# Kernel tuning notes

Measured on AMD Instinct MI355X. Metric: run time of the kernel, lower is better.

The kernel has to match this reference:

```python
import jax, jax.numpy as jnp
import numpy as np

D = 64        # state dim (num_output)
H = 256       # MLP hidden width
B = 4096      # batch
NUM_STEPS = 16  # fixed-step Dormand-Prince steps over t in [0,1] per bijector


def _mlp(t, y, W1, b1, W2, b2, W3, b3):
    # time-conditioned MLP: concat scalar t to state, two tanh layers, linear out
    tcol = jnp.full((y.shape[0], 1), t, dtype=y.dtype)
    h = jnp.tanh(jnp.concatenate([y, tcol], axis=1) @ W1 + b1)
    h = jnp.tanh(h @ W2 + b2)
    return h @ W3 + b3


def _dopri5_fixed(f, y0):
    # classic Dormand-Prince (RK45) Butcher tableau, 5th-order solution,
    # fixed step h = 1/NUM_STEPS from t=0 to t=1
    h = jnp.asarray(1.0 / NUM_STEPS, dtype=y0.dtype)

    def step(y, i):
        t = i.astype(y0.dtype) * h
        k1 = f(t, y)
        k2 = f(t + h * (1/5),  y + h * ((1/5) * k1))
        k3 = f(t + h * (3/10), y + h * ((3/40) * k1 + (9/40) * k2))
        k4 = f(t + h * (4/5),  y + h * ((44/45) * k1 - (56/15) * k2 + (32/9) * k3))
        k5 = f(t + h * (8/9),  y + h * ((19372/6561) * k1 - (25360/2187) * k2
                                        + (64448/6561) * k3 - (212/729) * k4))
        k6 = f(t + h,          y + h * ((9017/3168) * k1 - (355/33) * k2
                                        + (46732/5247) * k3 + (49/176) * k4
                                        - (5103/18656) * k5))
        y_next = y + h * ((35/384) * k1 + (500/1113) * k3 + (125/192) * k4
                          - (2187/6784) * k5 + (11/84) * k6)
        return y_next, None

    y_final, _ = jax.lax.scan(step, y0, jnp.arange(NUM_STEPS))
    return y_final


def setup_inputs() -> dict:
    key = jax.random.key(0)
    ks = jax.random.split(key, 7)
    s_in = 1.0 / np.sqrt(D + 1)
    s_h = 1.0 / np.sqrt(H)
    inp = {"x": jax.random.normal(ks[0], (B, D), dtype=jnp.float32)}
    for i, base in enumerate([1, 4]):
        inp[f"p{i}_W1"] = jax.random.normal(ks[base], (D + 1, H), dtype=jnp.float32) * s_in
        inp[f"p{i}_b1"] = jnp.zeros((H,), dtype=jnp.float32)
        inp[f"p{i}_W2"] = jax.random.normal(ks[base + 1], (H, H), dtype=jnp.float32) * s_h
        inp[f"p{i}_b2"] = jnp.zeros((H,), dtype=jnp.float32)
        inp[f"p{i}_W3"] = jax.random.normal(ks[base + 2], (H, D), dtype=jnp.float32) * s_h
        inp[f"p{i}_b3"] = jnp.zeros((D,), dtype=jnp.float32)
    return inp


def reference(x, p0_W1, p0_b1, p0_W2, p0_b2, p0_W3, p0_b3,
              p1_W1, p1_b1, p1_W2, p1_b2, p1_W3, p1_b3):
    # Chain(list(reversed(bijectors))).forward applies bijector 0 first, then 1.
    # FFJORD bijector forward = integrate dz/dt = mlp(t, z) from t=0 to t=1.
    y = x
    params = [(p0_W1, p0_b1, p0_W2, p0_b2, p0_W3, p0_b3),
              (p1_W1, p1_b1, p1_W2, p1_b2, p1_W3, p1_b3)]
    for (W1, b1, W2, b2, W3, b3) in params:
        f = lambda t, z: _mlp(t, z, W1, b1, W2, b2, W3, b3)
        y = _dopri5_fixed(f, y)
    return y
```

## Files before the change

### kernel.cpp

```cpp
#include <hip/hip_runtime.h>

typedef __attribute__((ext_vector_type(8))) short short8;
typedef __attribute__((ext_vector_type(4))) float f32x4;

#define MROWS 16
#define NSTEPS 16


__device__ __forceinline__ unsigned short bf16rne(float f) {
  unsigned int u = __float_as_uint(f);
  u += 0x7FFFu + ((u >> 16) & 1u);
  return (unsigned short)(u >> 16);
}

__device__ __forceinline__ float tanh_fast(float x) {
  x = fminf(12.0f, x);
  float e = __builtin_amdgcn_exp2f(x * 2.8853900817779268f);
  return __builtin_fmaf(-2.0f, __builtin_amdgcn_rcpf(e + 1.0f), 1.0f);
}

__global__ void ffjord_setup(const float* __restrict__ W1a, const float* __restrict__ W2a,
                             const float* __restrict__ W3a, const float* __restrict__ W1b,
                             const float* __restrict__ W2b, const float* __restrict__ W3b,
                             unsigned short* __restrict__ ws) {
  int gid = blockIdx.x * blockDim.x + threadIdx.x;
  int bij = gid / 12288;
  int r = gid - bij * 12288;
  const float* W1 = bij ? W1b : W1a;
  const float* W2 = bij ? W2b : W2a;
  const float* W3 = bij ? W3b : W3a;
  unsigned short* o = ws + bij * 98304;
  const float* src;
  int kstride;
  if (r < 2048) {
    int lane = r & 63, nt = (r >> 6) & 15, ks = r >> 10;
    int k0 = ks * 32 + (lane >> 4) * 8, n = nt * 16 + (lane & 15);
    src = W1 + k0 * 256 + n; kstride = 256; o += r * 8;
  } else if (r < 10240) {
    int rr = r - 2048;
    int lane = rr & 63, nt = (rr >> 6) & 15, ks = rr >> 10;
    int k0 = ks * 32 + (lane >> 4) * 8, n = nt * 16 + (lane & 15);
    src = W2 + k0 * 256 + n; kstride = 256; o += 16384 + rr * 8;
  } else {
    int rr = r - 10240;
    int lane = rr & 63, nt = (rr >> 6) & 3, ks = rr >> 8;
    int k0 = ks * 32 + (lane >> 4) * 8, n = nt * 16 + (lane & 15);
    src = W3 + k0 * 64 + n; kstride = 64; o += 81920 + rr * 8;
  }
  #pragma unroll
  for (int j = 0; j < 8; j++) o[j] = bf16rne(src[j * kstride]);
}

__global__ __launch_bounds__(512, 2) void ffjord_main(
    const float* __restrict__ x, float* __restrict__ out,
    const unsigned short* __restrict__ ws,
    const float* __restrict__ W1a, const float* __restrict__ b1a,
    const float* __restrict__ b2a, const float* __restrict__ b3a,
    const float* __restrict__ W1b, const float* __restrict__ b1b,
    const float* __restrict__ b2b, const float* __restrict__ b3b) {
  __shared__ __align__(16) unsigned short zA[1024];
  __shared__ __align__(16) unsigned short h1A[4096];
  __shared__ __align__(16) unsigned short h2A[4096];
  __shared__ __align__(16) float fbufA[16 * 68];
  __shared__ __align__(16) float fbufB[16 * 68];

  const int tid = threadIdx.x;
  const int wave = tid >> 6;
  const int lane = tid & 63;
  const int cl = lane & 15;
  const int qd = lane >> 4;
  const int w4 = wave & 3;
  const int ksb = (wave >> 2) * 4;
  const int row0 = blockIdx.x * MROWS;
  const int rown = tid >> 5;
  const int d0 = (tid & 31) * 2;

  const float hstep = 1.0f / 16.0f;

  float y[2];
  {
    float2 v = *(const float2*)(x + (row0 + rown) * 64 + d0);
    y[0] = v.x; y[1] = v.y;
  }
  float k[6][2];

  const int zoff = (d0 >> 5) * 512 + (rown + 16 * ((d0 & 31) >> 3)) * 8 + (d0 & 7);

  const float ACO[6][5] = {
      {0.f, 0.f, 0.f, 0.f, 0.f},
      {1.f / 5.f, 0.f, 0.f, 0.f, 0.f},
      {3.f / 40.f, 9.f / 40.f, 0.f, 0.f, 0.f},
      {44.f / 45.f, -56.f / 15.f, 32.f / 9.f, 0.f, 0.f},
      {19372.f / 6561.f, -25360.f / 2187.f, 64448.f / 6561.f, -212.f / 729.f, 0.f},
      {9017.f / 3168.f, -355.f / 33.f, 46732.f / 5247.f, 49.f / 176.f, -5103.f / 18656.f}};
  const float CT[6] = {0.0f, 0.2f, 0.3f, 0.8f, 8.0f / 9.0f, 1.0f};
  const float BW0 = 35.f / 384.f, BW2 = 500.f / 1113.f, BW3 = 125.f / 192.f,
              BW4 = -2187.f / 6784.f, BW5 = 11.f / 84.f;

  for (int bij = 0; bij < 2; bij++) {
    const unsigned short* wsb = ws + bij * 98304;
    const float* W1 = bij ? W1b : W1a;
    const float* b1 = bij ? b1b : b1a;
    const float* b2 = bij ? b2b : b2a;
    const float* b3 = bij ? b3b : b3a;

    float b1c[2], w1tc[2], b2r[2];
    #pragma unroll
    for (int j = 0; j < 2; j++) {
      int c = (wave * 2 + j) * 16 + cl;
      b1c[j] = b1[c];
      w1tc[j] = W1[64 * 256 + c];
      b2r[j] = b2[c];
    }
    float b3r = (wave < 4) ? b3[w4 * 16 + cl] : 0.0f;

    const short8* w1p = (const short8*)wsb;
    const short8* w2p = (const short8*)(wsb + 16384);
    const short8* w3p = (const short8*)(wsb + 81920);
    short8 w1f[2][2];
    #pragma unroll
    for (int ks = 0; ks < 2; ks++)
      #pragma unroll
      for (int j = 0; j < 2; j++)
        w1f[ks][j] = w1p[(ks * 16 + wave * 2 + j) * 64 + lane];
    short8 w2f[8][2];
    #pragma unroll
    for (int ks = 0; ks < 8; ks++)
      #pragma unroll
      for (int j = 0; j < 2; j++)
        w2f[ks][j] = w2p[(ks * 16 + wave * 2 + j) * 64 + lane];
    short8 w3f[4];
    #pragma unroll
    for (int kk = 0; kk < 4; kk++)
      w3f[kk] = w3p[((ksb + kk) * 4 + w4) * 64 + lane];

    for (int step = 0; step < NSTEPS; step++) {
      float stepf = (float)step;
      #pragma unroll
      for (int s = 0; s < 6; s++) {
        float ts = (stepf + CT[s]) * hstep;

        {
          float z0 = y[0], z1 = y[1];
          #pragma unroll
          for (int j = 0; j < 5; j++)
            if (j < s) {
              float a = hstep * ACO[s][j];
              z0 += a * k[j][0];
              z1 += a * k[j][1];
            }
          ushort2 p;
          p.x = bf16rne(z0); p.y = bf16rne(z1);
          *(ushort2*)(zA + zoff) = p;
        }
        __syncthreads();

        {
          short8 a0 = ((const short8*)zA)[lane];
          short8 a1 = ((const short8*)zA)[64 + lane];
          #pragma unroll
          for (int j = 0; j < 2; j++) {
            f32x4 acc = {0.f, 0.f, 0.f, 0.f};
            acc = __builtin_amdgcn_mfma_f32_16x16x32_bf16(a0, w1f[0][j], acc, 0, 0, 0);
            acc = __builtin_amdgcn_mfma_f32_16x16x32_bf16(a1, w1f[1][j], acc, 0, 0, 0);
            int c = (wave * 2 + j) * 16 + cl;
            float be = __builtin_fmaf(ts, w1tc[j], b1c[j]);
            int boff = (c >> 5) * 512 + ((c & 31) >> 3) * 128 + (c & 7);
            #pragma unroll
            for (int reg = 0; reg < 4; reg++)
              h1A[boff + (4 * qd + reg) * 8] = bf16rne(tanh_fast(acc[reg] + be));
          }
        }
        __syncthreads();

        {
          f32x4 zero = {0.f, 0.f, 0.f, 0.f};
          f32x4 acc2[2] = {zero, zero};
          #pragma unroll
          for (int ks = 0; ks < 8; ks++) {
            short8 a = ((const short8*)h1A)[ks * 64 + lane];
            acc2[0] = __builtin_amdgcn_mfma_f32_16x16x32_bf16(a, w2f[ks][0], acc2[0], 0, 0, 0);
            acc2[1] = __builtin_amdgcn_mfma_f32_16x16x32_bf16(a, w2f[ks][1], acc2[1], 0, 0, 0);
          }
          #pragma unroll
          for (int j = 0; j < 2; j++) {
            int c = (wave * 2 + j) * 16 + cl;
            int boff = (c >> 5) * 512 + ((c & 31) >> 3) * 128 + (c & 7);
            #pragma unroll
            for (int reg = 0; reg < 4; reg++)
              h2A[boff + (4 * qd + reg) * 8] = bf16rne(tanh_fast(acc2[j][reg] + b2r[j]));
          }
        }
        __syncthreads();

        {
          f32x4 acc3 = {0.f, 0.f, 0.f, 0.f};
          #pragma unroll
          for (int kk = 0; kk < 4; kk++) {
            short8 a = ((const short8*)h2A)[(ksb + kk) * 64 + lane];
            acc3 = __builtin_amdgcn_mfma_f32_16x16x32_bf16(a, w3f[kk], acc3, 0, 0, 0);
          }
          int c = w4 * 16 + cl;
          float* fb = (wave < 4) ? fbufA : fbufB;
          #pragma unroll
          for (int reg = 0; reg < 4; reg++)
            fb[(4 * qd + reg) * 68 + c] = acc3[reg] + b3r;
        }
        __syncthreads();

        {
          float2 va = *(const float2*)(fbufA + rown * 68 + d0);
          float2 vb = *(const float2*)(fbufB + rown * 68 + d0);
          k[s][0] = va.x + vb.x;
          k[s][1] = va.y + vb.y;
        }
      }

      #pragma unroll
      for (int i = 0; i < 2; i++) {
        float d = BW0 * k[0][i] + BW2 * k[2][i] + BW3 * k[3][i] +
                  BW4 * k[4][i] + BW5 * k[5][i];
        y[i] += hstep * d;
      }
    }
  }

  float2 o2; o2.x = y[0]; o2.y = y[1];
  *(float2*)(out + (row0 + rown) * 64 + d0) = o2;
}

extern "C" void kernel_launch(void* const* d_in, const int* in_sizes, int n_in,
                              void* d_out, int out_size, void* d_ws, size_t ws_size,
                              hipStream_t stream) {
  (void)in_sizes; (void)n_in; (void)out_size; (void)ws_size;
  const float* x   = (const float*)d_in[0];
  const float* W1a = (const float*)d_in[1];
  const float* b1a = (const float*)d_in[2];
  const float* W2a = (const float*)d_in[3];
  const float* b2a = (const float*)d_in[4];
  const float* W3a = (const float*)d_in[5];
  const float* b3a = (const float*)d_in[6];
  const float* W1b = (const float*)d_in[7];
  const float* b1b = (const float*)d_in[8];
  const float* W2b = (const float*)d_in[9];
  const float* b2b = (const float*)d_in[10];
  const float* W3b = (const float*)d_in[11];
  const float* b3b = (const float*)d_in[12];
  unsigned short* ws = (unsigned short*)d_ws;
  float* out = (float*)d_out;

  hipLaunchKernelGGL(ffjord_setup, dim3(96), dim3(256), 0, stream,
                     W1a, W2a, W3a, W1b, W2b, W3b, ws);
  hipLaunchKernelGGL(ffjord_main, dim3(256), dim3(512), 0, stream,
                     x, out, ws, W1a, b1a, b2a, b3a, W1b, b1b, b2b, b3b);
}
```

Baseline: 348.0 us.

## Swap MFMA operand order to transpose outputs, vectorize bf16 packing and LDS stores

Swaps the A/B operands of the MFMA calls so each lane holds four consecutive hidden columns of one row. This allows packed bf16 conversion (cvt_pk_bf16 when available) and 8-byte LDS stores in place of four scalar 2-byte stores. Biases and the time-column term are folded into the accumulator init, and the K-loops are split into two independent accumulator chains to shorten MFMA dependency latency. The z buffer is padded to reduce LDS bank conflicts. The tanh input clamp is removed, which risks inf/NaN for large positive inputs.

```diff
diff --git a/kernel.cpp b/kernel.cpp
--- a/kernel.cpp
+++ b/kernel.cpp
@@ -3,9 +3,7 @@
 typedef __attribute__((ext_vector_type(8))) short short8;
 typedef __attribute__((ext_vector_type(4))) float f32x4;
 
-#define MROWS 16
 #define NSTEPS 16
-
 
 __device__ __forceinline__ unsigned short bf16rne(float f) {
   unsigned int u = __float_as_uint(f);
@@ -13,8 +11,24 @@
   return (unsigned short)(u >> 16);
 }
 
+#if __has_builtin(__builtin_amdgcn_cvt_pk_bf16_f32)
+typedef __attribute__((ext_vector_type(2))) __bf16 v2bf16;
+__device__ __forceinline__ unsigned int pk2(float a, float b) {
+  v2bf16 t = __builtin_amdgcn_cvt_pk_bf16_f32(a, b);
+  unsigned int r;
+  __builtin_memcpy(&r, &t, 4);
+  return r;
+}
+#else
+__device__ __forceinline__ unsigned int pk2(float a, float b) {
+  unsigned int ua = __float_as_uint(a), ub = __float_as_uint(b);
+  ua += 0x7FFFu + ((ua >> 16) & 1u);
+  ub += 0x7FFFu + ((ub >> 16) & 1u);
+  return (ua >> 16) | (ub & 0xFFFF0000u);
+}
+#endif
+
 __device__ __forceinline__ float tanh_fast(float x) {
-  x = fminf(12.0f, x);
   float e = __builtin_amdgcn_exp2f(x * 2.8853900817779268f);
   return __builtin_fmaf(-2.0f, __builtin_amdgcn_rcpf(e + 1.0f), 1.0f);
 }
@@ -58,33 +72,41 @@
     const float* __restrict__ b2a, const float* __restrict__ b3a,
     const float* __restrict__ W1b, const float* __restrict__ b1b,
     const float* __restrict__ b2b, const float* __restrict__ b3b) {
-  __shared__ __align__(16) unsigned short zA[1024];
+  __shared__ __align__(16) unsigned short zA[1088];
   __shared__ __align__(16) unsigned short h1A[4096];
   __shared__ __align__(16) unsigned short h2A[4096];
-  __shared__ __align__(16) float fbufA[16 * 68];
-  __shared__ __align__(16) float fbufB[16 * 68];
+  __shared__ __align__(16) float fbuf[2][16 * 68];
 
   const int tid = threadIdx.x;
   const int wave = tid >> 6;
   const int lane = tid & 63;
   const int cl = lane & 15;
   const int qd = lane >> 4;
-  const int w4 = wave & 3;
-  const int ksb = (wave >> 2) * 4;
-  const int row0 = blockIdx.x * MROWS;
-  const int rown = tid >> 5;
+  const int kh = wave >> 2;
+  const int mt3 = wave & 3;
+  const int c3 = mt3 * 16 + qd * 4;
+  const int row0 = blockIdx.x * 16;
+  const int row = tid >> 5;
   const int d0 = (tid & 31) * 2;
+
+  const int zoff = ((d0 >> 5) * 4 + ((d0 >> 3) & 3)) * 136 + row * 8 + (d0 & 7);
+  const int zrb = qd * 136 + cl * 8;
+
+  int hoff[2];
+  #pragma unroll
+  for (int t = 0; t < 2; t++) {
+    int c0 = (wave * 2 + t) * 16 + qd * 4;
+    hoff[t] = (c0 >> 5) * 512 + ((c0 & 31) >> 3) * 128 + cl * 8 + (c0 & 7);
+  }
 
   const float hstep = 1.0f / 16.0f;
 
   float y[2];
   {
-    float2 v = *(const float2*)(x + (row0 + rown) * 64 + d0);
+    float2 v = *(const float2*)(x + (row0 + row) * 64 + d0);
     y[0] = v.x; y[1] = v.y;
   }
   float k[6][2];
-
-  const int zoff = (d0 >> 5) * 512 + (rown + 16 * ((d0 & 31) >> 3)) * 8 + (d0 & 7);
 
   const float ACO[6][5] = {
       {0.f, 0.f, 0.f, 0.f, 0.f},
@@ -104,15 +126,17 @@
     const float* b2 = bij ? b2b : b2a;
     const float* b3 = bij ? b3b : b3a;
 
-    float b1c[2], w1tc[2], b2r[2];
-    #pragma unroll
-    for (int j = 0; j < 2; j++) {
-      int c = (wave * 2 + j) * 16 + cl;
-      b1c[j] = b1[c];
-      w1tc[j] = W1[64 * 256 + c];
-      b2r[j] = b2[c];
+    f32x4 b1c[2], w1t4[2], b2c[2];
+    #pragma unroll
+    for (int t = 0; t < 2; t++) {
+      int c0 = (wave * 2 + t) * 16 + qd * 4;
+      b1c[t] = *(const f32x4*)(b1 + c0);
+      w1t4[t] = *(const f32x4*)(W1 + 64 * 256 + c0);
+      b2c[t] = *(const f32x4*)(b2 + c0);
     }
-    float b3r = (wave < 4) ? b3[w4 * 16 + cl] : 0.0f;
+    f32x4 b3c;
+    if (kh == 0) b3c = *(const f32x4*)(b3 + c3);
+    else { b3c[0] = 0.f; b3c[1] = 0.f; b3c[2] = 0.f; b3c[3] = 0.f; }
 
     const short8* w1p = (const short8*)wsb;
     const short8* w2p = (const short8*)(wsb + 16384);
@@ -121,18 +145,18 @@
     #pragma unroll
     for (int ks = 0; ks < 2; ks++)
       #pragma unroll
-      for (int j = 0; j < 2; j++)
-        w1f[ks][j] = w1p[(ks * 16 + wave * 2 + j) * 64 + lane];
+      for (int t = 0; t < 2; t++)
+        w1f[ks][t] = w1p[(ks * 16 + wave * 2 + t) * 64 + lane];
     short8 w2f[8][2];
     #pragma unroll
     for (int ks = 0; ks < 8; ks++)
       #pragma unroll
-      for (int j = 0; j < 2; j++)
-        w2f[ks][j] = w2p[(ks * 16 + wave * 2 + j) * 64 + lane];
+      for (int t = 0; t < 2; t++)
+        w2f[ks][t] = w2p[(ks * 16 + wave * 2 + t) * 64 + lane];
     short8 w3f[4];
     #pragma unroll
     for (int kk = 0; kk < 4; kk++)
-      w3f[kk] = w3p[((ksb + kk) * 4 + w4) * 64 + lane];
+      w3f[kk] = w3p[((kh * 4 + kk) * 4 + mt3) * 64 + lane];
 
     for (int step = 0; step < NSTEPS; step++) {
       float stepf = (float)step;
@@ -149,70 +173,81 @@
               z0 += a * k[j][0];
               z1 += a * k[j][1];
             }
-          ushort2 p;
-          p.x = bf16rne(z0); p.y = bf16rne(z1);
-          *(ushort2*)(zA + zoff) = p;
-        }
-        __syncthreads();
-
-        {
-          short8 a0 = ((const short8*)zA)[lane];
-          short8 a1 = ((const short8*)zA)[64 + lane];
-          #pragma unroll
-          for (int j = 0; j < 2; j++) {
-            f32x4 acc = {0.f, 0.f, 0.f, 0.f};
-            acc = __builtin_amdgcn_mfma_f32_16x16x32_bf16(a0, w1f[0][j], acc, 0, 0, 0);
-            acc = __builtin_amdgcn_mfma_f32_16x16x32_bf16(a1, w1f[1][j], acc, 0, 0, 0);
-            int c = (wave * 2 + j) * 16 + cl;
-            float be = __builtin_fmaf(ts, w1tc[j], b1c[j]);
-            int boff = (c >> 5) * 512 + ((c & 31) >> 3) * 128 + (c & 7);
+          *(unsigned int*)(zA + zoff) = pk2(z0, z1);
+        }
+        __syncthreads();
+
+        {
+          short8 a0 = *(const short8*)(zA + zrb);
+          short8 a1 = *(const short8*)(zA + zrb + 544);
+          #pragma unroll
+          for (int t = 0; t < 2; t++) {
+            f32x4 acc;
             #pragma unroll
-            for (int reg = 0; reg < 4; reg++)
-              h1A[boff + (4 * qd + reg) * 8] = bf16rne(tanh_fast(acc[reg] + be));
-          }
-        }
-        __syncthreads();
-
-        {
-          f32x4 zero = {0.f, 0.f, 0.f, 0.f};
-          f32x4 acc2[2] = {zero, zero};
-          #pragma unroll
-          for (int ks = 0; ks < 8; ks++) {
-            short8 a = ((const short8*)h1A)[ks * 64 + lane];
-            acc2[0] = __builtin_amdgcn_mfma_f32_16x16x32_bf16(a, w2f[ks][0], acc2[0], 0, 0, 0);
-            acc2[1] = __builtin_amdgcn_mfma_f32_16x16x32_bf16(a, w2f[ks][1], acc2[1], 0, 0, 0);
-          }
-          #pragma unroll
-          for (int j = 0; j < 2; j++) {
-            int c = (wave * 2 + j) * 16 + cl;
-            int boff = (c >> 5) * 512 + ((c & 31) >> 3) * 128 + (c & 7);
-            #pragma unroll
-            for (int reg = 0; reg < 4; reg++)
-              h2A[boff + (4 * qd + reg) * 8] = bf16rne(tanh_fast(acc2[j][reg] + b2r[j]));
-          }
-        }
-        __syncthreads();
-
-        {
-          f32x4 acc3 = {0.f, 0.f, 0.f, 0.f};
-          #pragma unroll
-          for (int kk = 0; kk < 4; kk++) {
-            short8 a = ((const short8*)h2A)[(ksb + kk) * 64 + lane];
-            acc3 = __builtin_amdgcn_mfma_f32_16x16x32_bf16(a, w3f[kk], acc3, 0, 0, 0);
-          }
-          int c = w4 * 16 + cl;
-          float* fb = (wave < 4) ? fbufA : fbufB;
-          #pragma unroll
-          for (int reg = 0; reg < 4; reg++)
-            fb[(4 * qd + reg) * 68 + c] = acc3[reg] + b3r;
-        }
-        __syncthreads();
-
-        {
-          float2 va = *(const float2*)(fbufA + rown * 68 + d0);
-          float2 vb = *(const float2*)(fbufB + rown * 68 + d0);
-          k[s][0] = va.x + vb.x;
-          k[s][1] = va.y + vb.y;
+            for (int r = 0; r < 4; r++)
+              acc[r] = __builtin_fmaf(ts, w1t4[t][r], b1c[t][r]);
+            acc = __builtin_amdgcn_mfma_f32_16x16x32_bf16(w1f[0][t], a0, acc, 0, 0, 0);
+            acc = __builtin_amdgcn_mfma_f32_16x16x32_bf16(w1f[1][t], a1, acc, 0, 0, 0);
+            uint2 pv;
+            pv.x = pk2(tanh_fast(acc[0]), tanh_fast(acc[1]));
+            pv.y = pk2(tanh_fast(acc[2]), tanh_fast(acc[3]));
+            *(uint2*)(h1A + hoff[t]) = pv;
+          }
+        }
+        __syncthreads();
+
+        {
+          f32x4 accA[2], accB[2];
+          #pragma unroll
+          for (int t = 0; t < 2; t++) {
+            accA[t] = b2c[t];
+            accB[t][0] = 0.f; accB[t][1] = 0.f; accB[t][2] = 0.f; accB[t][3] = 0.f;
+          }
+          #pragma unroll
+          for (int ks = 0; ks < 4; ks++) {
+            short8 hb = ((const short8*)h1A)[ks * 64 + lane];
+            accA[0] = __builtin_amdgcn_mfma_f32_16x16x32_bf16(w2f[ks][0], hb, accA[0], 0, 0, 0);
+            accA[1] = __builtin_amdgcn_mfma_f32_16x16x32_bf16(w2f[ks][1], hb, accA[1], 0, 0, 0);
+          }
+          #pragma unroll
+          for (int ks = 4; ks < 8; ks++) {
+            short8 hb = ((const short8*)h1A)[ks * 64 + lane];
+            accB[0] = __builtin_amdgcn_mfma_f32_16x16x32_bf16(w2f[ks][0], hb, accB[0], 0, 0, 0);
+            accB[1] = __builtin_amdgcn_mfma_f32_16x16x32_bf16(w2f[ks][1], hb, accB[1], 0, 0, 0);
+          }
+          #pragma unroll
+          for (int t = 0; t < 2; t++) {
+            uint2 pv;
+            pv.x = pk2(tanh_fast(accA[t][0] + accB[t][0]), tanh_fast(accA[t][1] + accB[t][1]));
+            pv.y = pk2(tanh_fast(accA[t][2] + accB[t][2]), tanh_fast(accA[t][3] + accB[t][3]));
+            *(uint2*)(h2A + hoff[t]) = pv;
+          }
+        }
+        __syncthreads();
+
+        {
+          f32x4 accP = b3c;
+          f32x4 accQ; accQ[0] = 0.f; accQ[1] = 0.f; accQ[2] = 0.f; accQ[3] = 0.f;
+          short8 hb0 = ((const short8*)h2A)[(kh * 4 + 0) * 64 + lane];
+          short8 hb1 = ((const short8*)h2A)[(kh * 4 + 1) * 64 + lane];
+          short8 hb2 = ((const short8*)h2A)[(kh * 4 + 2) * 64 + lane];
+          short8 hb3 = ((const short8*)h2A)[(kh * 4 + 3) * 64 + lane];
+          accP = __builtin_amdgcn_mfma_f32_16x16x32_bf16(w3f[0], hb0, accP, 0, 0, 0);
+          accP = __builtin_amdgcn_mfma_f32_16x16x32_bf16(w3f[1], hb1, accP, 0, 0, 0);
+          accQ = __builtin_amdgcn_mfma_f32_16x16x32_bf16(w3f[2], hb2, accQ, 0, 0, 0);
+          accQ = __builtin_amdgcn_mfma_f32_16x16x32_bf16(w3f[3], hb3, accQ, 0, 0, 0);
+          f32x4 res;
+          #pragma unroll
+          for (int r = 0; r < 4; r++) res[r] = accP[r] + accQ[r];
+          *(f32x4*)(&fbuf[kh][cl * 68 + c3]) = res;
+        }
+        __syncthreads();
+
+        {
+          float2 fa = *(const float2*)(&fbuf[0][row * 68 + d0]);
+          float2 fb = *(const float2*)(&fbuf[1][row * 68 + d0]);
+          k[s][0] = fa.x + fb.x;
+          k[s][1] = fa.y + fb.y;
         }
       }
 
@@ -226,7 +261,7 @@
   }
 
   float2 o2; o2.x = y[0]; o2.y = y[1];
-  *(float2*)(out + (row0 + rown) * 64 + d0) = o2;
+  *(float2*)(out + (row0 + row) * 64 + d0) = o2;
 }
 
 extern "C" void kernel_launch(void* const* d_in, const int* in_sizes, int n_in,
```

New measurement: 332.2 us. -4.5%, faster.
